# Performance work log

Measured on AMD Instinct MI355X. Metric: run time of the kernel, lower is better.

Reference implementation:

```python
import jax, jax.numpy as jnp
import numpy as np

DIM = 256
HEADS = 8
HEAD_DIM = DIM // HEADS  # 32
SCALE = HEAD_DIM ** -0.5
EPS = 1e-5


def _ternary_spike(x, vth):
    # x: [B,C,H,W], vth: [C] -> spikes in {-1,0,+1}
    v = vth[None, :, None, None]
    return jnp.where(x >= v, 1.0, 0.0) - jnp.where(x <= -v, 1.0, 0.0)


def setup_inputs() -> dict:
    key = jax.random.key(0)
    ks = jax.random.split(key, 5)
    B, C, H, W = 16, DIM, 64, 64
    s = C ** -0.5  # kaiming-ish scale for 1x1 conv weights
    return {
        "x": jax.random.normal(ks[0], (B, C, H, W), jnp.float32),
        "q_w": jax.random.normal(ks[1], (C, C), jnp.float32) * s,
        "k_w": jax.random.normal(ks[2], (C, C), jnp.float32) * s,
        "v_w": jax.random.normal(ks[3], (C, C), jnp.float32) * s,
        "proj_w": jax.random.normal(ks[4], (C, C), jnp.float32) * s,
        "bn_gamma": jnp.ones((C,), jnp.float32),
        "bn_beta": jnp.zeros((C,), jnp.float32),
        "q_vth": jnp.ones((C,), jnp.float32),
        "k_vth": jnp.ones((C,), jnp.float32),
    }


def reference(x, q_w, k_w, v_w, proj_w, bn_gamma, bn_beta, q_vth, k_vth):
    B, C, H, W = x.shape
    N = H * W
    # 1x1 convs == per-pixel channel matmuls
    q = jnp.einsum('oc,bchw->bohw', q_w, x)
    k = jnp.einsum('oc,bchw->bohw', k_w, x)
    v0 = jnp.einsum('oc,bchw->bohw', v_w, x)
    # BatchNorm2d (training-mode batch stats over B,H,W)
    mean = v0.mean(axis=(0, 2, 3))
    var = v0.var(axis=(0, 2, 3))
    v = (v0 - mean[None, :, None, None]) * jax.lax.rsqrt(var + EPS)[None, :, None, None]
    v = v * bn_gamma[None, :, None, None] + bn_beta[None, :, None, None]
    # ternary spiking activations on q, k
    qs = _ternary_spike(q, q_vth).reshape(B, HEADS, HEAD_DIM, N)
    ks_ = _ternary_spike(k, k_vth).reshape(B, HEADS, HEAD_DIM, N)
    vr = v.reshape(B, HEADS, HEAD_DIM, N)
    # channel-wise linear attention: [B,h,d,d] scores over spatial N
    attn = jax.nn.softmax(jnp.einsum('bhdn,bhen->bhde', qs, ks_) * SCALE, axis=-1)
    out = jnp.einsum('bhde,bhen->bhdn', attn, vr).reshape(B, C, H, W)
    return jnp.einsum('oc,bchw->bohw', proj_w, out) + x
```

## Files before the change

kernel.cpp:

```cpp
#include <hip/hip_runtime.h>
#include <hip/hip_bf16.h>
#include <stdint.h>
#include <math.h>

typedef __attribute__((ext_vector_type(4))) float f32x4;
typedef __attribute__((ext_vector_type(8))) short s16x8;

#define MFMA16(a,b,c) __builtin_amdgcn_mfma_f32_16x16x32_bf16((a),(b),(c),0,0,0)

#define Bc 16
#define Cc 256
#define Nc 4096
#define HDc 32
#define SCALE_F 0.17677669529663688f

__device__ __forceinline__ uint16_t f2bf(float x){
  uint32_t u = __float_as_uint(x);
  return (uint16_t)((u + 0x7fffu + ((u >> 16) & 1u)) >> 16);
}
__device__ __forceinline__ float bf2f(uint16_t b){
  return __uint_as_float(((uint32_t)b) << 16);
}

extern "C" __global__ __launch_bounds__(256) void k0_prep(
    const float* __restrict__ qw, const float* __restrict__ kw, const float* __restrict__ vw,
    uint16_t* __restrict__ qwh, uint16_t* __restrict__ qwl,
    uint16_t* __restrict__ kwh, uint16_t* __restrict__ kwl,
    uint16_t* __restrict__ vwb)
{
  int i = blockIdx.x * 256 + threadIdx.x;
  float q = qw[i]; uint16_t qh = f2bf(q);
  qwh[i] = qh; qwl[i] = f2bf(q - bf2f(qh));
  float k = kw[i]; uint16_t kh = f2bf(k);
  kwh[i] = kh; kwl[i] = f2bf(k - bf2f(kh));
  vwb[i] = f2bf(vw[i]);
}

extern "C" __global__ __launch_bounds__(256, 2) void k1_qkv(
    const float* __restrict__ x,
    const uint16_t* __restrict__ qwh, const uint16_t* __restrict__ qwl,
    const uint16_t* __restrict__ kwh, const uint16_t* __restrict__ kwl,
    const uint16_t* __restrict__ vwb,
    const float* __restrict__ qvth, const float* __restrict__ kvth,
    uint16_t* __restrict__ qs, uint16_t* __restrict__ ks,
    uint16_t* __restrict__ v0t,
    float* __restrict__ psum, float* __restrict__ psq)
{
  const int XP = 264;
  __shared__ __align__(16) uint16_t xhi[64 * 264];
  __shared__ __align__(16) uint16_t xlo[64 * 264];
  __shared__ float vthq_s[256];
  __shared__ float vthk_s[256];

  const int tid  = threadIdx.x;
  const int lane = tid & 63, wid = tid >> 6;
  const int l15  = lane & 15, lg = lane >> 4;
  const int nb = blockIdx.x, b = blockIdx.y;
  const int nbase = nb * 64;

  vthq_s[tid] = qvth[tid];
  vthk_s[tid] = kvth[tid];

  for (int kst = 0; kst < 2; ++kst){
    #pragma unroll
    for (int ni = 0; ni < 4; ++ni){
      const int n  = ni * 16 + l15;
      const int c0 = wid * 64 + kst * 32 + lg * 8;
      const float* xp = x + ((size_t)b * Cc + c0) * Nc + nbase + n;
      s16x8 vh, vl;
      #pragma unroll
      for (int j = 0; j < 8; ++j){
        float v = xp[(size_t)j * Nc];
        uint16_t h = f2bf(v);
        vh[j] = (short)h;
        vl[j] = (short)f2bf(v - bf2f(h));
      }
      const int a = n * XP + c0;
      *(s16x8*)&xhi[a] = vh;
      *(s16x8*)&xlo[a] = vl;
    }
  }
  __syncthreads();

  const int wrow = wid * 64;
  const f32x4 fz = {0.f, 0.f, 0.f, 0.f};

  f32x4 accq[4][4], acck[4][4];
  #pragma unroll
  for (int mi = 0; mi < 4; ++mi)
    #pragma unroll
    for (int ni = 0; ni < 4; ++ni){ accq[mi][ni] = fz; acck[mi][ni] = fz; }

  for (int kc = 0; kc < 256; kc += 32){
    s16x8 bh[4], bl[4];
    #pragma unroll
    for (int ni = 0; ni < 4; ++ni){
      const int a = (ni * 16 + l15) * XP + kc + lg * 8;
      bh[ni] = *(const s16x8*)&xhi[a];
      bl[ni] = *(const s16x8*)&xlo[a];
    }
    #pragma unroll
    for (int mi = 0; mi < 4; ++mi){
      const int wa = (wrow + mi * 16 + l15) * Cc + kc + lg * 8;
      s16x8 aqh = *(const s16x8*)&qwh[wa];
      s16x8 aql = *(const s16x8*)&qwl[wa];
      s16x8 akh = *(const s16x8*)&kwh[wa];
      s16x8 akl = *(const s16x8*)&kwl[wa];
      #pragma unroll
      for (int ni = 0; ni < 4; ++ni){
        accq[mi][ni] = MFMA16(aqh, bh[ni], accq[mi][ni]);
        accq[mi][ni] = MFMA16(aqh, bl[ni], accq[mi][ni]);
        accq[mi][ni] = MFMA16(aql, bh[ni], accq[mi][ni]);
        acck[mi][ni] = MFMA16(akh, bh[ni], acck[mi][ni]);
        acck[mi][ni] = MFMA16(akh, bl[ni], acck[mi][ni]);
        acck[mi][ni] = MFMA16(akl, bh[ni], acck[mi][ni]);
      }
    }
  }

  #pragma unroll
  for (int mi = 0; mi < 4; ++mi){
    #pragma unroll
    for (int r = 0; r < 4; ++r){
      const int o = wrow + mi * 16 + lg * 4 + r;
      const float vq = vthq_s[o], vk = vthk_s[o];
      uint16_t* qp = qs + ((size_t)b * Cc + o) * Nc + nbase;
      uint16_t* kp = ks + ((size_t)b * Cc + o) * Nc + nbase;
      #pragma unroll
      for (int ni = 0; ni < 4; ++ni){
        const float aq = accq[mi][ni][r];
        const float ak = acck[mi][ni][r];
        float sq = (aq >= vq ? 1.f : 0.f) - (aq <= -vq ? 1.f : 0.f);
        float sk = (ak >= vk ? 1.f : 0.f) - (ak <= -vk ? 1.f : 0.f);
        qp[ni * 16 + l15] = f2bf(sq);
        kp[ni * 16 + l15] = f2bf(sk);
      }
    }
  }

  f32x4 accv[4][4];
  #pragma unroll
  for (int mi = 0; mi < 4; ++mi)
    #pragma unroll
    for (int ni = 0; ni < 4; ++ni) accv[mi][ni] = fz;

  for (int kc = 0; kc < 256; kc += 32){
    s16x8 bh[4];
    #pragma unroll
    for (int ni = 0; ni < 4; ++ni)
      bh[ni] = *(const s16x8*)&xhi[(ni * 16 + l15) * XP + kc + lg * 8];
    #pragma unroll
    for (int mi = 0; mi < 4; ++mi){
      s16x8 av = *(const s16x8*)&vwb[(wrow + mi * 16 + l15) * Cc + kc + lg * 8];
      #pragma unroll
      for (int ni = 0; ni < 4; ++ni)
        accv[mi][ni] = MFMA16(av, bh[ni], accv[mi][ni]);
    }
  }

  const int bid = b * 64 + nb;
  #pragma unroll
  for (int mi = 0; mi < 4; ++mi){
    #pragma unroll
    for (int r = 0; r < 4; ++r){
      float s1 = 0.f, s2 = 0.f;
      #pragma unroll
      for (int ni = 0; ni < 4; ++ni){
        const float v = accv[mi][ni][r];
        s1 += v; s2 += v * v;
      }
      #pragma unroll
      for (int mk = 1; mk < 16; mk <<= 1){
        s1 += __shfl_xor(s1, mk);
        s2 += __shfl_xor(s2, mk);
      }
      if (l15 == 0){
        const int o = wrow + mi * 16 + lg * 4 + r;
        psum[(size_t)bid * Cc + o] = s1;
        psq [(size_t)bid * Cc + o] = s2;
      }
    }
  }

  float* scr = (float*)xhi + wid * (64 * 20);
  for (int mi = 0; mi < 4; ++mi){
    __syncthreads();
    #pragma unroll
    for (int ni = 0; ni < 4; ++ni)
      *(f32x4*)&scr[(ni * 16 + l15) * 20 + lg * 4] = accv[mi][ni];
    __syncthreads();
    const float* sp = scr + lane * 20;
    s16x8 o0, o1;
    #pragma unroll
    for (int j = 0; j < 8; ++j){
      o0[j] = (short)f2bf(sp[j]);
      o1[j] = (short)f2bf(sp[8 + j]);
    }
    uint16_t* dst = v0t + ((size_t)b * Nc + nbase + lane) * Cc + wrow + mi * 16;
    *(s16x8*)dst = o0;
    *(s16x8*)(dst + 8) = o1;
  }
}

extern "C" __global__ __launch_bounds__(256) void k2_stats(
    const float* __restrict__ psum, const float* __restrict__ psq,
    const float* __restrict__ gamma, const float* __restrict__ beta,
    float* __restrict__ sc, float* __restrict__ sh)
{
  const int c = threadIdx.x;
  float s1 = 0.f, s2 = 0.f;
  for (int i = 0; i < 1024; ++i){
    s1 += psum[i * 256 + c];
    s2 += psq [i * 256 + c];
  }
  const float inv = 1.f / 65536.f;
  const float mean = s1 * inv;
  const float var  = s2 * inv - mean * mean;
  const float s = gamma[c] * rsqrtf(var + 1e-5f);
  sc[c] = s;
  sh[c] = beta[c] - mean * s;
}

extern "C" __global__ __launch_bounds__(512, 2) void k3_attn(
    const uint16_t* __restrict__ qs, const uint16_t* __restrict__ ks,
    const float* __restrict__ pw, const float* __restrict__ sc, const float* __restrict__ sh,
    float* __restrict__ Mp, float* __restrict__ bias)
{
  __shared__ float Spart[8][32 * 33];
  __shared__ float Sf[32 * 33];
  __shared__ __align__(16) uint16_t attn_t[32 * 40];

  const int h = blockIdx.x, b = blockIdx.y;
  const int tid = threadIdx.x;
  const int lane = tid & 63, w = tid >> 6;
  const int l15 = lane & 15, lg = lane >> 4;

  const f32x4 fz = {0.f, 0.f, 0.f, 0.f};
  f32x4 acc[2][2] = {{fz, fz}, {fz, fz}};
  const uint16_t* qb = qs + ((size_t)b * Cc + h * HDc) * Nc;
  const uint16_t* kb = ks + ((size_t)b * Cc + h * HDc) * Nc;
  const int n0base = w * 512;
  for (int n0 = n0base; n0 < n0base + 512; n0 += 32){
    const int off = n0 + lg * 8;
    s16x8 a0 = *(const s16x8*)&qb[(l15) * Nc + off];
    s16x8 a1 = *(const s16x8*)&qb[(16 + l15) * Nc + off];
    s16x8 b0 = *(const s16x8*)&kb[(l15) * Nc + off];
    s16x8 b1 = *(const s16x8*)&kb[(16 + l15) * Nc + off];
    acc[0][0] = MFMA16(a0, b0, acc[0][0]);
    acc[0][1] = MFMA16(a0, b1, acc[0][1]);
    acc[1][0] = MFMA16(a1, b0, acc[1][0]);
    acc[1][1] = MFMA16(a1, b1, acc[1][1]);
  }
  #pragma unroll
  for (int di = 0; di < 2; ++di)
    #pragma unroll
    for (int ei = 0; ei < 2; ++ei)
      #pragma unroll
      for (int r = 0; r < 4; ++r)
        Spart[w][(di * 16 + lg * 4 + r) * 33 + ei * 16 + l15] = acc[di][ei][r];
  __syncthreads();

  for (int e = tid; e < 1024; e += 512){
    const int row = e >> 5, col = e & 31;
    float s = 0.f;
    #pragma unroll
    for (int ww = 0; ww < 8; ++ww) s += Spart[ww][row * 33 + col];
    Sf[row * 33 + col] = s * SCALE_F;
  }
  __syncthreads();

  if (tid < 32){
    const int d = tid;
    float mx = -1e30f;
    #pragma unroll
    for (int e = 0; e < 32; ++e) mx = fmaxf(mx, Sf[d * 33 + e]);
    float p[32]; float sum = 0.f;
    #pragma unroll
    for (int e = 0; e < 32; ++e){ p[e] = expf(Sf[d * 33 + e] - mx); sum += p[e]; }
    const float inv = 1.f / sum;
    #pragma unroll
    for (int e = 0; e < 32; ++e) attn_t[e * 40 + d] = f2bf(p[e] * inv);
  }
  __syncthreads();

  s16x8 bfr[2];
  #pragma unroll
  for (int ei = 0; ei < 2; ++ei)
    bfr[ei] = *(const s16x8*)&attn_t[(ei * 16 + l15) * 40 + lg * 8];

  f32x4 m[2][2] = {{fz, fz}, {fz, fz}};
  #pragma unroll
  for (int mi = 0; mi < 2; ++mi){
    const float* ap = pw + ((size_t)(w * 32 + mi * 16 + l15)) * Cc + h * HDc + lg * 8;
    f32x4 a0 = *(const f32x4*)ap;
    f32x4 a1 = *(const f32x4*)(ap + 4);
    s16x8 af;
    #pragma unroll
    for (int j = 0; j < 4; ++j){ af[j] = (short)f2bf(a0[j]); af[4 + j] = (short)f2bf(a1[j]); }
    #pragma unroll
    for (int ei = 0; ei < 2; ++ei)
      m[mi][ei] = MFMA16(af, bfr[ei], m[mi][ei]);
  }

  const float sc0 = sc[h * HDc + l15],      sc1 = sc[h * HDc + 16 + l15];
  const float sh0 = sh[h * HDc + l15],      sh1 = sh[h * HDc + 16 + l15];
  #pragma unroll
  for (int mi = 0; mi < 2; ++mi){
    #pragma unroll
    for (int r = 0; r < 4; ++r){
      const int o = w * 32 + mi * 16 + lg * 4 + r;
      float* mp = Mp + ((size_t)b * Cc + o) * Cc + h * HDc;
      const float m0 = m[mi][0][r], m1 = m[mi][1][r];
      mp[l15]      = m0 * sc0;
      mp[16 + l15] = m1 * sc1;
      float bb = m0 * sh0 + m1 * sh1;
      #pragma unroll
      for (int mk = 1; mk < 16; mk <<= 1) bb += __shfl_xor(bb, mk);
      if (l15 == 0) atomicAdd(&bias[b * Cc + o], bb);
    }
  }
}

extern "C" __global__ __launch_bounds__(256, 2) void k4_proj(
    const float* __restrict__ Mp, const uint16_t* __restrict__ v0t,
    const float* __restrict__ bias, const float* __restrict__ x,
    float* __restrict__ out)
{
  const int tid = threadIdx.x;
  const int lane = tid & 63, wid = tid >> 6;
  const int l15 = lane & 15, lg = lane >> 4;
  const int nb = blockIdx.x, b = blockIdx.y;
  const int nbase = nb * 64, wrow = wid * 64;

  const f32x4 fz = {0.f, 0.f, 0.f, 0.f};
  f32x4 acc[4][4];
  #pragma unroll
  for (int mi = 0; mi < 4; ++mi)
    #pragma unroll
    for (int ni = 0; ni < 4; ++ni) acc[mi][ni] = fz;

  for (int kc = 0; kc < 256; kc += 32){
    s16x8 bf[4];
    #pragma unroll
    for (int ni = 0; ni < 4; ++ni)
      bf[ni] = *(const s16x8*)&v0t[((size_t)b * Nc + nbase + ni * 16 + l15) * Cc + kc + lg * 8];
    #pragma unroll
    for (int mi = 0; mi < 4; ++mi){
      const float* ap = Mp + ((size_t)b * Cc + wrow + mi * 16 + l15) * Cc + kc + lg * 8;
      f32x4 a0 = *(const f32x4*)ap;
      f32x4 a1 = *(const f32x4*)(ap + 4);
      s16x8 af;
      #pragma unroll
      for (int j = 0; j < 4; ++j){ af[j] = (short)f2bf(a0[j]); af[4 + j] = (short)f2bf(a1[j]); }
      #pragma unroll
      for (int ni = 0; ni < 4; ++ni)
        acc[mi][ni] = MFMA16(af, bf[ni], acc[mi][ni]);
    }
  }

  #pragma unroll
  for (int mi = 0; mi < 4; ++mi){
    #pragma unroll
    for (int r = 0; r < 4; ++r){
      const int o = wrow + mi * 16 + lg * 4 + r;
      const float bb = bias[b * Cc + o];
      const size_t base = ((size_t)b * Cc + o) * Nc + nbase;
      #pragma unroll
      for (int ni = 0; ni < 4; ++ni){
        const size_t aidx = base + ni * 16 + l15;
        out[aidx] = acc[mi][ni][r] + bb + x[aidx];
      }
    }
  }
}

extern "C" void kernel_launch(void* const* d_in, const int* in_sizes, int n_in,
                              void* d_out, int out_size, void* d_ws, size_t ws_size,
                              hipStream_t stream)
{
  (void)in_sizes; (void)n_in; (void)out_size; (void)ws_size;
  const float* x      = (const float*)d_in[0];
  const float* q_w    = (const float*)d_in[1];
  const float* k_w    = (const float*)d_in[2];
  const float* v_w    = (const float*)d_in[3];
  const float* proj_w = (const float*)d_in[4];
  const float* gamma  = (const float*)d_in[5];
  const float* beta   = (const float*)d_in[6];
  const float* q_vth  = (const float*)d_in[7];
  const float* k_vth  = (const float*)d_in[8];
  float* out = (float*)d_out;

  char* ws = (char*)d_ws;
  uint16_t* qwh = (uint16_t*)(ws + 0);
  uint16_t* qwl = (uint16_t*)(ws + 131072);
  uint16_t* kwh = (uint16_t*)(ws + 262144);
  uint16_t* kwl = (uint16_t*)(ws + 393216);
  uint16_t* vwb = (uint16_t*)(ws + 524288);
  uint16_t* v0t = (uint16_t*)(ws + 655360);
  float* psum   = (float*)(ws + 34209792);
  float* psq    = (float*)(ws + 35258368);
  float* sc     = (float*)(ws + 36306944);
  float* sh     = (float*)(ws + 36307968);
  float* Mp     = (float*)(ws + 36308992);
  float* bias   = (float*)(ws + 40503296);

  uint16_t* qs = (uint16_t*)d_out;
  uint16_t* ks = (uint16_t*)((char*)d_out + 33554432);

  hipMemsetAsync(bias, 0, 16 * 256 * sizeof(float), stream);

  k0_prep<<<256, 256, 0, stream>>>(q_w, k_w, v_w, qwh, qwl, kwh, kwl, vwb);
  k1_qkv<<<dim3(64, 16), 256, 0, stream>>>(x, qwh, qwl, kwh, kwl, vwb,
                                           q_vth, k_vth, qs, ks, v0t, psum, psq);
  k2_stats<<<1, 256, 0, stream>>>(psum, psq, gamma, beta, sc, sh);
  k3_attn<<<dim3(8, 16), 512, 0, stream>>>(qs, ks, proj_w, sc, sh, Mp, bias);
  k4_proj<<<dim3(64, 16), 256, 0, stream>>>(Mp, v0t, bias, x, out);
}
```

Measured before the change: 331.1 us.

## Split QKV and attention kernels across more blocks, parallelize BN stats, bf16 Mp

The QKV projection kernel now tiles 32 pixels by 128 output channels per block with a swizzled LDS layout and occupancy hint 4. Spike outputs are written as vectorized 16-byte stores through an LDS transpose. BN stats are reduced by 256 blocks over a channel-major partial-sum layout instead of a single block. The QK^T reduction is split over 8 spatial chunks in a separate kernel that stages data through LDS, and the softmax/projection kernel writes the fused matrix as bf16 so the final projection reads half the bytes. This adds kernels and the recomputation of the x load per output-channel half, in exchange for far more parallelism in the previously serialized stages.

```diff
diff --git a/kernel.cpp b/kernel.cpp
--- a/kernel.cpp
+++ b/kernel.cpp
@@ -8,10 +8,8 @@
 
 #define MFMA16(a,b,c) __builtin_amdgcn_mfma_f32_16x16x32_bf16((a),(b),(c),0,0,0)
 
-#define Bc 16
 #define Cc 256
 #define Nc 4096
-#define HDc 32
 #define SCALE_F 0.17677669529663688f
 
 __device__ __forceinline__ uint16_t f2bf(float x){
@@ -36,7 +34,7 @@
   vwb[i] = f2bf(vw[i]);
 }
 
-extern "C" __global__ __launch_bounds__(256, 2) void k1_qkv(
+extern "C" __global__ __launch_bounds__(256, 4) void k1_qkv(
     const float* __restrict__ x,
     const uint16_t* __restrict__ qwh, const uint16_t* __restrict__ qwl,
     const uint16_t* __restrict__ kwh, const uint16_t* __restrict__ kwl,
@@ -46,27 +44,31 @@
     uint16_t* __restrict__ v0t,
     float* __restrict__ psum, float* __restrict__ psq)
 {
-  const int XP = 264;
-  __shared__ __align__(16) uint16_t xhi[64 * 264];
-  __shared__ __align__(16) uint16_t xlo[64 * 264];
-  __shared__ float vthq_s[256];
-  __shared__ float vthk_s[256];
+  __shared__ __align__(16) uint16_t XS[16384];
+  __shared__ float vq_s[128];
+  __shared__ float vk_s[128];
 
   const int tid  = threadIdx.x;
   const int lane = tid & 63, wid = tid >> 6;
   const int l15  = lane & 15, lg = lane >> 4;
-  const int nb = blockIdx.x, b = blockIdx.y;
-  const int nbase = nb * 64;
-
-  vthq_s[tid] = qvth[tid];
-  vthk_s[tid] = kvth[tid];
-
-  for (int kst = 0; kst < 2; ++kst){
-    #pragma unroll
-    for (int ni = 0; ni < 4; ++ni){
-      const int n  = ni * 16 + l15;
+  const int nb = blockIdx.x, oh = blockIdx.y, b = blockIdx.z;
+  const int OH = oh * 128;
+  const int wrow = OH + wid * 32;
+  const int nbase = nb * 32;
+
+  if (tid < 128) vq_s[tid] = qvth[OH + tid];
+  else           vk_s[tid - 128] = kvth[OH + tid - 128];
+
+  uint16_t* XH = XS;
+  uint16_t* XL = XS + 8192;
+
+  #pragma unroll
+  for (int ni_s = 0; ni_s < 2; ++ni_s){
+    #pragma unroll
+    for (int kst = 0; kst < 2; ++kst){
+      const int n  = ni_s * 16 + l15;
       const int c0 = wid * 64 + kst * 32 + lg * 8;
-      const float* xp = x + ((size_t)b * Cc + c0) * Nc + nbase + n;
+      const float* xp = x + ((size_t)(b * Cc + c0)) * Nc + nbase + n;
       s16x8 vh, vl;
       #pragma unroll
       for (int j = 0; j < 8; ++j){
@@ -75,39 +77,38 @@
         vh[j] = (short)h;
         vl[j] = (short)f2bf(v - bf2f(h));
       }
-      const int a = n * XP + c0;
-      *(s16x8*)&xhi[a] = vh;
-      *(s16x8*)&xlo[a] = vl;
-    }
-  }
-  __syncthreads();
-
-  const int wrow = wid * 64;
+      const int U = ((wid * 2 + kst) * 2 + ni_s) * 64 + l15 + lg * 16;
+      *(s16x8*)&XH[U * 8] = vh;
+      *(s16x8*)&XL[U * 8] = vl;
+    }
+  }
+  __syncthreads();
+
   const f32x4 fz = {0.f, 0.f, 0.f, 0.f};
 
-  f32x4 accq[4][4], acck[4][4];
-  #pragma unroll
-  for (int mi = 0; mi < 4; ++mi)
-    #pragma unroll
-    for (int ni = 0; ni < 4; ++ni){ accq[mi][ni] = fz; acck[mi][ni] = fz; }
+  f32x4 accq[2][2], acck[2][2];
+  #pragma unroll
+  for (int mi = 0; mi < 2; ++mi)
+    #pragma unroll
+    for (int ni = 0; ni < 2; ++ni){ accq[mi][ni] = fz; acck[mi][ni] = fz; }
 
   for (int kc = 0; kc < 256; kc += 32){
-    s16x8 bh[4], bl[4];
-    #pragma unroll
-    for (int ni = 0; ni < 4; ++ni){
-      const int a = (ni * 16 + l15) * XP + kc + lg * 8;
-      bh[ni] = *(const s16x8*)&xhi[a];
-      bl[ni] = *(const s16x8*)&xlo[a];
-    }
-    #pragma unroll
-    for (int mi = 0; mi < 4; ++mi){
+    const int g = kc >> 5;
+    s16x8 bh[2], bl[2];
+    #pragma unroll
+    for (int ni = 0; ni < 2; ++ni){
+      bh[ni] = *(const s16x8*)&XH[((g * 2 + ni) * 64 + lane) * 8];
+      bl[ni] = *(const s16x8*)&XL[((g * 2 + ni) * 64 + lane) * 8];
+    }
+    #pragma unroll
+    for (int mi = 0; mi < 2; ++mi){
       const int wa = (wrow + mi * 16 + l15) * Cc + kc + lg * 8;
       s16x8 aqh = *(const s16x8*)&qwh[wa];
       s16x8 aql = *(const s16x8*)&qwl[wa];
       s16x8 akh = *(const s16x8*)&kwh[wa];
       s16x8 akl = *(const s16x8*)&kwl[wa];
       #pragma unroll
-      for (int ni = 0; ni < 4; ++ni){
+      for (int ni = 0; ni < 2; ++ni){
         accq[mi][ni] = MFMA16(aqh, bh[ni], accq[mi][ni]);
         accq[mi][ni] = MFMA16(aqh, bl[ni], accq[mi][ni]);
         accq[mi][ni] = MFMA16(aql, bh[ni], accq[mi][ni]);
@@ -117,55 +118,81 @@
       }
     }
   }
-
-  #pragma unroll
-  for (int mi = 0; mi < 4; ++mi){
-    #pragma unroll
-    for (int r = 0; r < 4; ++r){
-      const int o = wrow + mi * 16 + lg * 4 + r;
-      const float vq = vthq_s[o], vk = vthk_s[o];
-      uint16_t* qp = qs + ((size_t)b * Cc + o) * Nc + nbase;
-      uint16_t* kp = ks + ((size_t)b * Cc + o) * Nc + nbase;
-      #pragma unroll
-      for (int ni = 0; ni < 4; ++ni){
-        const float aq = accq[mi][ni][r];
-        const float ak = acck[mi][ni][r];
-        float sq = (aq >= vq ? 1.f : 0.f) - (aq <= -vq ? 1.f : 0.f);
-        float sk = (ak >= vk ? 1.f : 0.f) - (ak <= -vk ? 1.f : 0.f);
-        qp[ni * 16 + l15] = f2bf(sq);
-        kp[ni * 16 + l15] = f2bf(sk);
-      }
-    }
-  }
-
-  f32x4 accv[4][4];
-  #pragma unroll
-  for (int mi = 0; mi < 4; ++mi)
-    #pragma unroll
-    for (int ni = 0; ni < 4; ++ni) accv[mi][ni] = fz;
+  __syncthreads();
+
+  {
+    float* sscr = (float*)XL + wid * (16 * 36);
+    const int o_ = lane >> 2;
+    const int nloc = (lane & 3) * 8;
+    #pragma unroll
+    for (int mi = 0; mi < 2; ++mi){
+      const int o = wrow + mi * 16 + o_;
+      #pragma unroll
+      for (int ni = 0; ni < 2; ++ni)
+        #pragma unroll
+        for (int r = 0; r < 4; ++r)
+          sscr[(lg * 4 + r) * 36 + ni * 16 + l15] = accq[mi][ni][r];
+      {
+        const float* sp = sscr + o_ * 36 + nloc;
+        const float vq = vq_s[o - OH];
+        s16x8 pk;
+        #pragma unroll
+        for (int j = 0; j < 8; ++j){
+          float v = sp[j];
+          float s = (v >= vq ? 1.f : 0.f) - (v <= -vq ? 1.f : 0.f);
+          pk[j] = (short)f2bf(s);
+        }
+        *(s16x8*)&qs[((size_t)(b * Cc + o)) * Nc + nbase + nloc] = pk;
+      }
+      #pragma unroll
+      for (int ni = 0; ni < 2; ++ni)
+        #pragma unroll
+        for (int r = 0; r < 4; ++r)
+          sscr[(lg * 4 + r) * 36 + ni * 16 + l15] = acck[mi][ni][r];
+      {
+        const float* sp = sscr + o_ * 36 + nloc;
+        const float vk = vk_s[o - OH];
+        s16x8 pk;
+        #pragma unroll
+        for (int j = 0; j < 8; ++j){
+          float v = sp[j];
+          float s = (v >= vk ? 1.f : 0.f) - (v <= -vk ? 1.f : 0.f);
+          pk[j] = (short)f2bf(s);
+        }
+        *(s16x8*)&ks[((size_t)(b * Cc + o)) * Nc + nbase + nloc] = pk;
+      }
+    }
+  }
+
+  f32x4 accv[2][2];
+  #pragma unroll
+  for (int mi = 0; mi < 2; ++mi)
+    #pragma unroll
+    for (int ni = 0; ni < 2; ++ni) accv[mi][ni] = fz;
 
   for (int kc = 0; kc < 256; kc += 32){
-    s16x8 bh[4];
-    #pragma unroll
-    for (int ni = 0; ni < 4; ++ni)
-      bh[ni] = *(const s16x8*)&xhi[(ni * 16 + l15) * XP + kc + lg * 8];
-    #pragma unroll
-    for (int mi = 0; mi < 4; ++mi){
+    const int g = kc >> 5;
+    s16x8 bh[2];
+    #pragma unroll
+    for (int ni = 0; ni < 2; ++ni)
+      bh[ni] = *(const s16x8*)&XH[((g * 2 + ni) * 64 + lane) * 8];
+    #pragma unroll
+    for (int mi = 0; mi < 2; ++mi){
       s16x8 av = *(const s16x8*)&vwb[(wrow + mi * 16 + l15) * Cc + kc + lg * 8];
       #pragma unroll
-      for (int ni = 0; ni < 4; ++ni)
+      for (int ni = 0; ni < 2; ++ni)
         accv[mi][ni] = MFMA16(av, bh[ni], accv[mi][ni]);
     }
   }
 
-  const int bid = b * 64 + nb;
-  #pragma unroll
-  for (int mi = 0; mi < 4; ++mi){
+  const int bid = b * 128 + nb;
+  #pragma unroll
+  for (int mi = 0; mi < 2; ++mi){
     #pragma unroll
     for (int r = 0; r < 4; ++r){
       float s1 = 0.f, s2 = 0.f;
       #pragma unroll
-      for (int ni = 0; ni < 4; ++ni){
+      for (int ni = 0; ni < 2; ++ni){
         const float v = accv[mi][ni][r];
         s1 += v; s2 += v * v;
       }
@@ -176,27 +203,30 @@
       }
       if (l15 == 0){
         const int o = wrow + mi * 16 + lg * 4 + r;
-        psum[(size_t)bid * Cc + o] = s1;
-        psq [(size_t)bid * Cc + o] = s2;
-      }
-    }
-  }
-
-  float* scr = (float*)xhi + wid * (64 * 20);
-  for (int mi = 0; mi < 4; ++mi){
-    __syncthreads();
-    #pragma unroll
-    for (int ni = 0; ni < 4; ++ni)
-      *(f32x4*)&scr[(ni * 16 + l15) * 20 + lg * 4] = accv[mi][ni];
-    __syncthreads();
-    const float* sp = scr + lane * 20;
+        psum[(size_t)o * 2048 + bid] = s1;
+        psq [(size_t)o * 2048 + bid] = s2;
+      }
+    }
+  }
+  __syncthreads();
+
+  {
+    float* tscr = (float*)XS + wid * (32 * 36);
+    #pragma unroll
+    for (int mi = 0; mi < 2; ++mi)
+      #pragma unroll
+      for (int ni = 0; ni < 2; ++ni)
+        #pragma unroll
+        for (int r = 0; r < 4; ++r)
+          tscr[(mi * 16 + lg * 4 + r) * 36 + ni * 16 + l15] = accv[mi][ni][r];
+    const int n = lane >> 1, half = lane & 1;
     s16x8 o0, o1;
     #pragma unroll
-    for (int j = 0; j < 8; ++j){
-      o0[j] = (short)f2bf(sp[j]);
-      o1[j] = (short)f2bf(sp[8 + j]);
-    }
-    uint16_t* dst = v0t + ((size_t)b * Nc + nbase + lane) * Cc + wrow + mi * 16;
+    for (int k = 0; k < 8; ++k){
+      o0[k] = (short)f2bf(tscr[(half * 16 + k) * 36 + n]);
+      o1[k] = (short)f2bf(tscr[(half * 16 + 8 + k) * 36 + n]);
+    }
+    uint16_t* dst = v0t + ((size_t)(b * Nc + nbase + n)) * Cc + wrow + half * 16;
     *(s16x8*)dst = o0;
     *(s16x8*)(dst + 8) = o1;
   }
@@ -207,26 +237,101 @@
     const float* __restrict__ gamma, const float* __restrict__ beta,
     float* __restrict__ sc, float* __restrict__ sh)
 {
-  const int c = threadIdx.x;
-  float s1 = 0.f, s2 = 0.f;
-  for (int i = 0; i < 1024; ++i){
-    s1 += psum[i * 256 + c];
-    s2 += psq [i * 256 + c];
-  }
-  const float inv = 1.f / 65536.f;
-  const float mean = s1 * inv;
-  const float var  = s2 * inv - mean * mean;
-  const float s = gamma[c] * rsqrtf(var + 1e-5f);
-  sc[c] = s;
-  sh[c] = beta[c] - mean * s;
-}
-
-extern "C" __global__ __launch_bounds__(512, 2) void k3_attn(
+  __shared__ float w1[4], w2[4];
+  const int c = blockIdx.x;
+  const int tid = threadIdx.x;
+  const float* p1 = psum + (size_t)c * 2048 + tid * 8;
+  const float* p2 = psq  + (size_t)c * 2048 + tid * 8;
+  f32x4 a0 = *(const f32x4*)p1,  a1 = *(const f32x4*)(p1 + 4);
+  f32x4 b0 = *(const f32x4*)p2,  b1 = *(const f32x4*)(p2 + 4);
+  float s1 = a0[0]+a0[1]+a0[2]+a0[3] + a1[0]+a1[1]+a1[2]+a1[3];
+  float s2 = b0[0]+b0[1]+b0[2]+b0[3] + b1[0]+b1[1]+b1[2]+b1[3];
+  #pragma unroll
+  for (int mk = 1; mk < 64; mk <<= 1){
+    s1 += __shfl_xor(s1, mk);
+    s2 += __shfl_xor(s2, mk);
+  }
+  if ((tid & 63) == 0){ w1[tid >> 6] = s1; w2[tid >> 6] = s2; }
+  __syncthreads();
+  if (tid == 0){
+    float t1 = w1[0]+w1[1]+w1[2]+w1[3];
+    float t2 = w2[0]+w2[1]+w2[2]+w2[3];
+    const float inv = 1.f / 65536.f;
+    const float mean = t1 * inv;
+    const float var  = t2 * inv - mean * mean;
+    const float s = gamma[c] * rsqrtf(var + 1e-5f);
+    sc[c] = s;
+    sh[c] = beta[c] - mean * s;
+  }
+}
+
+extern "C" __global__ __launch_bounds__(256) void k3a_qk(
     const uint16_t* __restrict__ qs, const uint16_t* __restrict__ ks,
-    const float* __restrict__ pw, const float* __restrict__ sc, const float* __restrict__ sh,
-    float* __restrict__ Mp, float* __restrict__ bias)
-{
-  __shared__ float Spart[8][32 * 33];
+    float* __restrict__ Sbuf)
+{
+  __shared__ __align__(16) uint16_t QK[18432];
+  const int h = blockIdx.x, b = blockIdx.y, ns = blockIdx.z;
+  const int tid = threadIdx.x;
+  const int lane = tid & 63, w = tid >> 6;
+
+  uint16_t* qlds = QK;
+  uint16_t* klds = QK + 8192;
+
+  const f32x4 fz = {0.f, 0.f, 0.f, 0.f};
+  f32x4 acc[2][2] = {{fz, fz}, {fz, fz}};
+  const uint16_t* qb = qs + ((size_t)(b * Cc + h * 32)) * Nc;
+  const uint16_t* kb = ks + ((size_t)(b * Cc + h * 32)) * Nc;
+
+  const int row = tid & 31, seg = tid >> 5;
+  for (int cc = 0; cc < 2; ++cc){
+    const int n0 = ns * 512 + cc * 256;
+    const uint16_t* qsrc = qb + (size_t)row * Nc + n0 + seg * 32;
+    const uint16_t* ksrc = kb + (size_t)row * Nc + n0 + seg * 32;
+    #pragma unroll
+    for (int i = 0; i < 4; ++i){
+      const int U = (seg * 2 + (row >> 4)) * 64 + (row & 15) + i * 16;
+      *(s16x8*)&qlds[U * 8] = *(const s16x8*)(qsrc + i * 8);
+      *(s16x8*)&klds[U * 8] = *(const s16x8*)(ksrc + i * 8);
+    }
+    __syncthreads();
+    #pragma unroll
+    for (int kci = 0; kci < 2; ++kci){
+      const int g = w * 2 + kci;
+      s16x8 a0 = *(const s16x8*)&qlds[((g * 2 + 0) * 64 + lane) * 8];
+      s16x8 a1 = *(const s16x8*)&qlds[((g * 2 + 1) * 64 + lane) * 8];
+      s16x8 b0 = *(const s16x8*)&klds[((g * 2 + 0) * 64 + lane) * 8];
+      s16x8 b1 = *(const s16x8*)&klds[((g * 2 + 1) * 64 + lane) * 8];
+      acc[0][0] = MFMA16(a0, b0, acc[0][0]);
+      acc[0][1] = MFMA16(a0, b1, acc[0][1]);
+      acc[1][0] = MFMA16(a1, b0, acc[1][0]);
+      acc[1][1] = MFMA16(a1, b1, acc[1][1]);
+    }
+    __syncthreads();
+  }
+
+  float* Sp = (float*)QK;
+  const int l15 = lane & 15, lg = lane >> 4;
+  #pragma unroll
+  for (int di = 0; di < 2; ++di)
+    #pragma unroll
+    for (int ei = 0; ei < 2; ++ei)
+      #pragma unroll
+      for (int r = 0; r < 4; ++r)
+        Sp[w * 1056 + (di * 16 + lg * 4 + r) * 33 + ei * 16 + l15] = acc[di][ei][r];
+  __syncthreads();
+  for (int idx = tid; idx < 1024; idx += 256){
+    const int d = idx >> 5, e = idx & 31;
+    float s = Sp[0 * 1056 + d * 33 + e] + Sp[1 * 1056 + d * 33 + e]
+            + Sp[2 * 1056 + d * 33 + e] + Sp[3 * 1056 + d * 33 + e];
+    Sbuf[((size_t)(ns * 128 + b * 8 + h)) * 1024 + idx] = s;
+  }
+}
+
+extern "C" __global__ __launch_bounds__(256) void k3b_sm(
+    const float* __restrict__ Sbuf, const float* __restrict__ pw,
+    const float* __restrict__ sc, const float* __restrict__ sh,
+    uint16_t* __restrict__ Mp16, float* __restrict__ bias)
+{
   __shared__ float Sf[32 * 33];
   __shared__ __align__(16) uint16_t attn_t[32 * 40];
 
@@ -235,37 +340,12 @@
   const int lane = tid & 63, w = tid >> 6;
   const int l15 = lane & 15, lg = lane >> 4;
 
-  const f32x4 fz = {0.f, 0.f, 0.f, 0.f};
-  f32x4 acc[2][2] = {{fz, fz}, {fz, fz}};
-  const uint16_t* qb = qs + ((size_t)b * Cc + h * HDc) * Nc;
-  const uint16_t* kb = ks + ((size_t)b * Cc + h * HDc) * Nc;
-  const int n0base = w * 512;
-  for (int n0 = n0base; n0 < n0base + 512; n0 += 32){
-    const int off = n0 + lg * 8;
-    s16x8 a0 = *(const s16x8*)&qb[(l15) * Nc + off];
-    s16x8 a1 = *(const s16x8*)&qb[(16 + l15) * Nc + off];
-    s16x8 b0 = *(const s16x8*)&kb[(l15) * Nc + off];
-    s16x8 b1 = *(const s16x8*)&kb[(16 + l15) * Nc + off];
-    acc[0][0] = MFMA16(a0, b0, acc[0][0]);
-    acc[0][1] = MFMA16(a0, b1, acc[0][1]);
-    acc[1][0] = MFMA16(a1, b0, acc[1][0]);
-    acc[1][1] = MFMA16(a1, b1, acc[1][1]);
-  }
-  #pragma unroll
-  for (int di = 0; di < 2; ++di)
-    #pragma unroll
-    for (int ei = 0; ei < 2; ++ei)
-      #pragma unroll
-      for (int r = 0; r < 4; ++r)
-        Spart[w][(di * 16 + lg * 4 + r) * 33 + ei * 16 + l15] = acc[di][ei][r];
-  __syncthreads();
-
-  for (int e = tid; e < 1024; e += 512){
-    const int row = e >> 5, col = e & 31;
+  for (int idx = tid; idx < 1024; idx += 256){
     float s = 0.f;
     #pragma unroll
-    for (int ww = 0; ww < 8; ++ww) s += Spart[ww][row * 33 + col];
-    Sf[row * 33 + col] = s * SCALE_F;
+    for (int ns = 0; ns < 8; ++ns)
+      s += Sbuf[((size_t)(ns * 128 + b * 8 + h)) * 1024 + idx];
+    Sf[(idx >> 5) * 33 + (idx & 31)] = s * SCALE_F;
   }
   __syncthreads();
 
@@ -288,10 +368,12 @@
   for (int ei = 0; ei < 2; ++ei)
     bfr[ei] = *(const s16x8*)&attn_t[(ei * 16 + l15) * 40 + lg * 8];
 
-  f32x4 m[2][2] = {{fz, fz}, {fz, fz}};
-  #pragma unroll
-  for (int mi = 0; mi < 2; ++mi){
-    const float* ap = pw + ((size_t)(w * 32 + mi * 16 + l15)) * Cc + h * HDc + lg * 8;
+  const f32x4 fz = {0.f, 0.f, 0.f, 0.f};
+  f32x4 m[4][2];
+  #pragma unroll
+  for (int mi = 0; mi < 4; ++mi){
+    m[mi][0] = fz; m[mi][1] = fz;
+    const float* ap = pw + ((size_t)(w * 64 + mi * 16 + l15)) * Cc + h * 32 + lg * 8;
     f32x4 a0 = *(const f32x4*)ap;
     f32x4 a1 = *(const f32x4*)(ap + 4);
     s16x8 af;
@@ -302,17 +384,17 @@
       m[mi][ei] = MFMA16(af, bfr[ei], m[mi][ei]);
   }
 
-  const float sc0 = sc[h * HDc + l15],      sc1 = sc[h * HDc + 16 + l15];
-  const float sh0 = sh[h * HDc + l15],      sh1 = sh[h * HDc + 16 + l15];
-  #pragma unroll
-  for (int mi = 0; mi < 2; ++mi){
+  const float sc0 = sc[h * 32 + l15],      sc1 = sc[h * 32 + 16 + l15];
+  const float sh0 = sh[h * 32 + l15],      sh1 = sh[h * 32 + 16 + l15];
+  #pragma unroll
+  for (int mi = 0; mi < 4; ++mi){
     #pragma unroll
     for (int r = 0; r < 4; ++r){
-      const int o = w * 32 + mi * 16 + lg * 4 + r;
-      float* mp = Mp + ((size_t)b * Cc + o) * Cc + h * HDc;
+      const int o = w * 64 + mi * 16 + lg * 4 + r;
+      uint16_t* mp = Mp16 + ((size_t)(b * Cc + o)) * Cc + h * 32;
       const float m0 = m[mi][0][r], m1 = m[mi][1][r];
-      mp[l15]      = m0 * sc0;
-      mp[16 + l15] = m1 * sc1;
+      mp[l15]      = f2bf(m0 * sc0);
+      mp[16 + l15] = f2bf(m1 * sc1);
       float bb = m0 * sh0 + m1 * sh1;
       #pragma unroll
       for (int mk = 1; mk < 16; mk <<= 1) bb += __shfl_xor(bb, mk);
@@ -322,7 +404,7 @@
 }
 
 extern "C" __global__ __launch_bounds__(256, 2) void k4_proj(
-    const float* __restrict__ Mp, const uint16_t* __restrict__ v0t,
+    const uint16_t* __restrict__ Mp16, const uint16_t* __restrict__ v0t,
     const float* __restrict__ bias, const float* __restrict__ x,
     float* __restrict__ out)
 {
@@ -343,15 +425,10 @@
     s16x8 bf[4];
     #pragma unroll
     for (int ni = 0; ni < 4; ++ni)
-      bf[ni] = *(const s16x8*)&v0t[((size_t)b * Nc + nbase + ni * 16 + l15) * Cc + kc + lg * 8];
+      bf[ni] = *(const s16x8*)&v0t[((size_t)(b * Nc + nbase + ni * 16 + l15)) * Cc + kc + lg * 8];
     #pragma unroll
     for (int mi = 0; mi < 4; ++mi){
-      const float* ap = Mp + ((size_t)b * Cc + wrow + mi * 16 + l15) * Cc + kc + lg * 8;
-      f32x4 a0 = *(const f32x4*)ap;
-      f32x4 a1 = *(const f32x4*)(ap + 4);
-      s16x8 af;
-      #pragma unroll
-      for (int j = 0; j < 4; ++j){ af[j] = (short)f2bf(a0[j]); af[4 + j] = (short)f2bf(a1[j]); }
+      s16x8 af = *(const s16x8*)&Mp16[((size_t)(b * Cc + wrow + mi * 16 + l15)) * Cc + kc + lg * 8];
       #pragma unroll
       for (int ni = 0; ni < 4; ++ni)
         acc[mi][ni] = MFMA16(af, bf[ni], acc[mi][ni]);
@@ -364,7 +441,7 @@
     for (int r = 0; r < 4; ++r){
       const int o = wrow + mi * 16 + lg * 4 + r;
       const float bb = bias[b * Cc + o];
-      const size_t base = ((size_t)b * Cc + o) * Nc + nbase;
+      const size_t base = ((size_t)(b * Cc + o)) * Nc + nbase;
       #pragma unroll
       for (int ni = 0; ni < 4; ++ni){
         const size_t aidx = base + ni * 16 + l15;
@@ -398,10 +475,11 @@
   uint16_t* vwb = (uint16_t*)(ws + 524288);
   uint16_t* v0t = (uint16_t*)(ws + 655360);
   float* psum   = (float*)(ws + 34209792);
-  float* psq    = (float*)(ws + 35258368);
-  float* sc     = (float*)(ws + 36306944);
-  float* sh     = (float*)(ws + 36307968);
-  float* Mp     = (float*)(ws + 36308992);
+  float* psq    = (float*)(ws + 36306944);
+  float* Sbuf   = (float*)(ws + 34209792);
+  float* sc     = (float*)(ws + 38404096);
+  float* sh     = (float*)(ws + 38405120);
+  uint16_t* Mp16= (uint16_t*)(ws + 38406144);
   float* bias   = (float*)(ws + 40503296);
 
   uint16_t* qs = (uint16_t*)d_out;
@@ -410,9 +488,10 @@
   hipMemsetAsync(bias, 0, 16 * 256 * sizeof(float), stream);
 
   k0_prep<<<256, 256, 0, stream>>>(q_w, k_w, v_w, qwh, qwl, kwh, kwl, vwb);
-  k1_qkv<<<dim3(64, 16), 256, 0, stream>>>(x, qwh, qwl, kwh, kwl, vwb,
-                                           q_vth, k_vth, qs, ks, v0t, psum, psq);
-  k2_stats<<<1, 256, 0, stream>>>(psum, psq, gamma, beta, sc, sh);
-  k3_attn<<<dim3(8, 16), 512, 0, stream>>>(qs, ks, proj_w, sc, sh, Mp, bias);
-  k4_proj<<<dim3(64, 16), 256, 0, stream>>>(Mp, v0t, bias, x, out);
-}
+  k1_qkv<<<dim3(128, 2, 16), 256, 0, stream>>>(x, qwh, qwl, kwh, kwl, vwb,
+                                               q_vth, k_vth, qs, ks, v0t, psum, psq);
+  k2_stats<<<256, 256, 0, stream>>>(psum, psq, gamma, beta, sc, sh);
+  k3a_qk<<<dim3(8, 16, 8), 256, 0, stream>>>(qs, ks, Sbuf);
+  k3b_sm<<<dim3(8, 16), 256, 0, stream>>>(Sbuf, proj_w, sc, sh, Mp16, bias);
+  k4_proj<<<dim3(64, 16), 256, 0, stream>>>(Mp16, v0t, bias, x, out);
+}
```

Result: slower. 367.4 us (+10.9%).
